# Performance work log

Hardware: AMD Instinct MI355X
Metric: run time of the kernel (lower is better)

The kernel has to match this reference:

```python
import jax, jax.numpy as jnp
import numpy as np

N_HEAD = 12
SCALING = 0.17677669529663687  # 1/sqrt(head_dim=32)


def setup_inputs() -> dict:
    key = jax.random.key(0)
    ks = jax.random.split(key, 6)
    B, R, C, E = 1, 256, 384, 384
    s = 1.0 / np.sqrt(E)
    return {
        "x": jax.random.normal(ks[0], (B, R, C, E), dtype=jnp.float32),
        "Wq": (jax.random.normal(ks[1], (E, E), dtype=jnp.float32) * s),
        "Wk": (jax.random.normal(ks[2], (E, E), dtype=jnp.float32) * s),
        "Wv": (jax.random.normal(ks[3], (E, E), dtype=jnp.float32) * s),
        "Wq_s": (jax.random.normal(ks[4], (E, E), dtype=jnp.float32) * s),
        "Wk_s": (jax.random.normal(ks[5], (E, E), dtype=jnp.float32) * s),
        "res_mask": jnp.ones((B, C), dtype=jnp.int32),
        "seq_mask": jnp.ones((B, R), dtype=jnp.int32),
    }


def reference(x, Wq, Wk, Wv, Wq_s, Wk_s, res_mask, seq_mask):
    B, R, C, E = x.shape
    H = N_HEAD
    D = E // H
    NEG = jnp.finfo(x.dtype).min

    # ---- SeqWeightAttention: per-column attention over rows, query = row 0 ----
    scale_s = 1.0 / np.sqrt(D)
    msa = jnp.transpose(x, (0, 2, 1, 3))                 # [B,C,R,E]
    q0 = msa[:, :, 0]                                    # [B,C,E]
    Qs = (q0 @ Wq_s).reshape(B, C, 1, H, D)
    Qs = jnp.transpose(Qs, (0, 1, 3, 2, 4)) * scale_s    # [B,C,H,1,D]
    Ks = (msa @ Wk_s).reshape(B, C, R, H, D)
    Ks = jnp.transpose(Ks, (0, 1, 3, 4, 2))              # [B,C,H,D,R]
    QKs = Qs @ Ks                                        # [B,C,H,1,R]
    QKs = jnp.where(seq_mask[:, None, None, None, :] == 0, NEG, QKs)
    sw = jax.nn.softmax(QKs, axis=-1)
    sw = jnp.transpose(sw, (0, 4, 1, 2, 3))              # [B,R,C,H,1]

    # ---- main attention, row-contracted (attn_seq_weight path) ----
    scaling = SCALING / np.sqrt(C)                        # seqlen_scaling=True
    Q = (x @ Wq).reshape(B, R, C, H, D) * scaling * sw    # Q modulated by seq weights
    K = (x @ Wk).reshape(B, R, C, H, D)
    V = (x @ Wv).reshape(B, R, C, H, D)

    QK = jnp.einsum('brihd,brjhd->bhij', Q, K)            # contract rows + head_dim
    rm = res_mask[:, :, None] * res_mask[:, None, :]      # [B,C,C]
    QK = jnp.where(rm[:, None, :, :] == 0, NEG, QK)
    attn = jax.nn.softmax(QK, axis=-1)                    # [B,H,C,C]

    out = jnp.einsum('bhij,brjhd->brihd', attn, V)
    return out.reshape(B, R, C, E)
```

## Files before the change

### kernel.cpp

```cpp
#include <hip/hip_runtime.h>
#include <math.h>
#include <stdint.h>

#define DEV_INLINE __device__ __forceinline__

constexpr int R_ = 256, C_ = 384, E_ = 384, H_ = 12, D_ = 32;
constexpr float NEGF = -3.402823466e38f;

typedef __attribute__((ext_vector_type(4))) float f32x4;
typedef __attribute__((ext_vector_type(8))) short short8;
typedef __attribute__((ext_vector_type(4))) unsigned short u16x4;

constexpr size_t o_qs     = 0;
constexpr size_t o_p      = o_qs + (size_t)C_ * E_;
constexpr size_t o_logits = o_p + (size_t)C_ * H_ * E_;
constexpr size_t o_sw     = o_logits + (size_t)C_ * H_ * R_;
constexpr size_t o_attn   = o_sw + (size_t)C_ * H_ * R_;
constexpr size_t o_q3     = o_attn + (size_t)H_ * C_ * C_;
constexpr size_t SZBIG  = 75497472;
constexpr size_t ob_q3b = o_q3 * 4;
constexpr size_t ob_k3b = ob_q3b + SZBIG;
constexpr size_t ob_v3b = ob_k3b + SZBIG;
constexpr size_t ob_xb  = ob_v3b + SZBIG;
constexpr size_t QKSZ   = 7077888;

DEV_INLINE unsigned short bf16h(float x) {
  unsigned int u = __builtin_bit_cast(unsigned int, x);
  unsigned int r = (u + 0x7FFFu + ((u >> 16) & 1u)) >> 16;
  return (unsigned short)r;
}
DEV_INLINE float waveRedMax(float v) {
#pragma unroll
  for (int o = 32; o > 0; o >>= 1) v = fmaxf(v, __shfl_down(v, o));
  return v;
}
DEV_INLINE float waveRedSum(float v) {
#pragma unroll
  for (int o = 32; o > 0; o >>= 1) v += __shfl_down(v, o);
  return v;
}

DEV_INLINE void gll16(const void* g, void* l) {
  __builtin_amdgcn_global_load_lds(
      reinterpret_cast<__attribute__((address_space(1))) void*>(
          reinterpret_cast<uintptr_t>(g)),
      reinterpret_cast<__attribute__((address_space(3))) void*>(
          reinterpret_cast<uintptr_t>(l)),
      16, 0, 0);
}

template <int ROWS, int UPR, int MASK, int SHIFT>
DEV_INLINE void stageT(const unsigned short* __restrict__ g, int lda,
                       unsigned short* l) {
  int t = threadIdx.x, w = t >> 6, lane = t & 63;
  constexpr int NI = (ROWS * UPR) / 64;
  constexpr int PW = NI / 4;
#pragma unroll
  for (int j = 0; j < PW; ++j) {
    int u0 = (w * PW + j) * 64;
    int u = u0 + lane;
    int row = u / UPR, qp = u % UPR;
    int q = qp ^ ((row >> SHIFT) & MASK);
    gll16(g + (size_t)row * lda + q * 8, l + (size_t)u0 * 8);
  }
}

template <int MASK, int SHIFT>
DEV_INLINE short8 fragLd(const unsigned short* base, int row, int q, int rowShorts) {
  int qp = q ^ ((row >> SHIFT) & MASK);
  return *(const short8*)(base + row * rowShorts + qp * 8);
}

__global__ void k_qs(const float* __restrict__ x, const float* __restrict__ Wq_s,
                     float* __restrict__ ws) {
  int c = blockIdx.x, t = threadIdx.x;
  __shared__ float xl[E_];
  xl[t] = x[(size_t)c * E_ + t];
  __syncthreads();
  float s = 0.f;
#pragma unroll 8
  for (int k = 0; k < E_; ++k) s += xl[k] * Wq_s[(size_t)k * E_ + t];
  ws[o_qs + (size_t)c * E_ + t] = s * 0.17677669529663687f;
}

__global__ void k_p(const float* __restrict__ Wk_s, const float* __restrict__ ws,
                    unsigned short* __restrict__ Pb) {
  int h = blockIdx.x, c = blockIdx.y, t = threadIdx.x;
  __shared__ float q[D_];
  float s = 0.f;
  if (h < 12) {
    if (t < D_) q[t] = ws[o_qs + (size_t)c * E_ + h * D_ + t];
    __syncthreads();
    const float* wrow = &Wk_s[(size_t)t * E_ + h * D_];
#pragma unroll
    for (int d = 0; d < D_; d += 4) {
      float4 w = *(const float4*)&wrow[d];
      s += w.x * q[d] + w.y * q[d + 1] + w.z * q[d + 2] + w.w * q[d + 3];
    }
  }
  Pb[((size_t)c * 16 + h) * 384 + t] = bf16h(s);
}

__global__ __launch_bounds__(256) void k_logits_sm(
    const unsigned short* __restrict__ xb, const unsigned short* __restrict__ Pb,
    const int* __restrict__ seq_mask, float* __restrict__ swT) {
  int c = blockIdx.x, t = threadIdx.x;
  __shared__ unsigned short sA[256 * 32];
  __shared__ unsigned short sB[16 * 32];
  __shared__ float lg[12 * 256];
  __shared__ float red[4];
  int w = t >> 6, lane = t & 63, id16 = lane & 15, g = lane >> 4;
  f32x4 acc[4];
#pragma unroll
  for (int mi = 0; mi < 4; ++mi) acc[mi] = (f32x4){0.f, 0.f, 0.f, 0.f};

  for (int k0 = 0; k0 < 384; k0 += 32) {
    stageT<256, 4, 3, 0>(xb + (size_t)c * 384 + k0, 384 * 384, sA);
    if (w == 0) {
      int row = lane >> 2, qp = lane & 3, q = qp ^ (row & 3);
      gll16(Pb + ((size_t)c * 16 + row) * 384 + k0 + q * 8, sB);
    }
    __syncthreads();
    short8 Bf = fragLd<3, 0>(sB, id16, g, 32);
#pragma unroll
    for (int mi = 0; mi < 4; ++mi) {
      short8 Af = fragLd<3, 0>(sA, w * 64 + mi * 16 + id16, g, 32);
      acc[mi] = __builtin_amdgcn_mfma_f32_16x16x32_bf16(Af, Bf, acc[mi], 0, 0, 0);
    }
    __syncthreads();
  }
  int l4 = (lane >> 4) * 4;
#pragma unroll
  for (int mi = 0; mi < 4; ++mi) {
    if (id16 < 12) {
      f32x4 a = acc[mi];
#pragma unroll
      for (int reg = 0; reg < 4; ++reg)
        lg[id16 * 256 + w * 64 + mi * 16 + l4 + reg] = a[reg];
    }
  }
  __syncthreads();
  int wid = t >> 6;
  const float scal = 0.17677669529663687f / sqrtf((float)C_);
  bool masked = (seq_mask[t] == 0);
  for (int h = 0; h < 12; ++h) {
    float v = masked ? NEGF : lg[h * 256 + t];
    float m = waveRedMax(v);
    if ((t & 63) == 0) red[wid] = m;
    __syncthreads();
    float mx = fmaxf(fmaxf(red[0], red[1]), fmaxf(red[2], red[3]));
    __syncthreads();
    float e = expf(v - mx);
    float s = waveRedSum(e);
    if ((t & 63) == 0) red[wid] = s;
    __syncthreads();
    float sum = red[0] + red[1] + red[2] + red[3];
    swT[((size_t)h * 256 + t) * 384 + c] = e / sum * scal;
    __syncthreads();
  }
}

__global__ void k_cvt_x(const float* __restrict__ x, unsigned short* __restrict__ xb) {
  size_t i = ((size_t)blockIdx.x * 256 + threadIdx.x) * 16;
  unsigned short h[16];
#pragma unroll
  for (int j = 0; j < 4; ++j) {
    float4 f = *(const float4*)&x[i + j * 4];
    h[j * 4 + 0] = bf16h(f.x);
    h[j * 4 + 1] = bf16h(f.y);
    h[j * 4 + 2] = bf16h(f.z);
    h[j * 4 + 3] = bf16h(f.w);
  }
  *(short8*)&xb[i] = *(const short8*)&h[0];
  *(short8*)&xb[i + 8] = *(const short8*)&h[8];
}

__global__ void k_cvt_w(const float* __restrict__ Wq, const float* __restrict__ Wk,
                        const float* __restrict__ Wv, unsigned short* __restrict__ Wtb) {
  int n = blockIdx.x, k = threadIdx.x;
  const float* W;
  int col;
  if (n < 384)      { W = Wq; col = n; }
  else if (n < 768) { W = Wk; col = n - 384; }
  else              { W = Wv; col = n - 768; }
  Wtb[(size_t)n * 384 + k] = bf16h(W[(size_t)k * 384 + col]);
}

__global__ __launch_bounds__(256, 4) void k_proj_all(
    const unsigned short* __restrict__ xb, const unsigned short* __restrict__ Wtb,
    const float* __restrict__ swT, unsigned short* __restrict__ Q3b,
    unsigned short* __restrict__ K3b, unsigned short* __restrict__ V3b) {
  __shared__ __align__(16) unsigned short smem[2 * 128 * 64];
  unsigned short* sA = smem;
  unsigned short* sB = smem + 128 * 64;
  int Dd = blockIdx.x;
  int L = (Dd & 7) * 864 + (Dd >> 3);
  int bm = L / 9, bn = L - bm * 9;
  int n0 = bn * 128, m0 = bm * 128;
  int wave = threadIdx.x >> 6, wr = wave >> 1, wc = wave & 1;
  int lane = threadIdx.x & 63, id16 = lane & 15, g = lane >> 4;
  f32x4 acc[4][4];
#pragma unroll
  for (int mi = 0; mi < 4; ++mi)
#pragma unroll
    for (int ni = 0; ni < 4; ++ni) acc[mi][ni] = (f32x4){0.f, 0.f, 0.f, 0.f};

  for (int it = 0; it < 6; ++it) {
    stageT<128, 8, 7, 0>(xb + (size_t)m0 * 384 + it * 64, 384, sA);
    stageT<128, 8, 7, 0>(Wtb + (size_t)n0 * 384 + it * 64, 384, sB);
    __syncthreads();
    short8 Af[4][2], Bf[4][2];
#pragma unroll
    for (int mi = 0; mi < 4; ++mi) {
      int row = wr * 64 + mi * 16 + id16;
#pragma unroll
      for (int kk = 0; kk < 2; ++kk) Af[mi][kk] = fragLd<7, 0>(sA, row, kk * 4 + g, 64);
    }
#pragma unroll
    for (int ni = 0; ni < 4; ++ni) {
      int col = wc * 64 + ni * 16 + id16;
#pragma unroll
      for (int kk = 0; kk < 2; ++kk) Bf[ni][kk] = fragLd<7, 0>(sB, col, kk * 4 + g, 64);
    }
#pragma unroll
    for (int kk = 0; kk < 2; ++kk)
#pragma unroll
      for (int mi = 0; mi < 4; ++mi)
#pragma unroll
        for (int ni = 0; ni < 4; ++ni)
          acc[mi][ni] = __builtin_amdgcn_mfma_f32_16x16x32_bf16(Af[mi][kk], Bf[ni][kk],
                                                                acc[mi][ni], 0, 0, 0);
    __syncthreads();
  }

  int l4 = (lane >> 4) * 4;
  int r = bm / 3, cb = (bm % 3) * 128;
  if (bn < 6) {
    bool isQ = bn < 3;
    int hbase = isQ ? bn * 4 : (bn - 3) * 4;
#pragma unroll
    for (int mi = 0; mi < 4; ++mi) {
      int clBase = wr * 64 + mi * 16 + l4;
#pragma unroll
      for (int ni = 0; ni < 4; ++ni) {
        int nl = wc * 64 + ni * 16 + id16;
        int hhl = nl >> 5, d = nl & 31;
        f32x4 a = acc[mi][ni];
        if (isQ) {
          float4 sv =
              *(const float4*)&swT[((size_t)(hbase + hhl) * 256 + r) * 384 + cb + clBase];
          a[0] *= sv.x; a[1] *= sv.y; a[2] *= sv.z; a[3] *= sv.w;
        }
#pragma unroll
        for (int reg = 0; reg < 4; ++reg)
          smem[hhl * 4096 + (clBase + reg) * 32 + d] = bf16h(a[reg]);
      }
    }
    __syncthreads();
    unsigned short* dst = isQ ? Q3b : K3b;
#pragma unroll
    for (int seg = 0; seg < 8; ++seg) {
      int off = seg * 2048 + threadIdx.x * 8;
      int hhl = off >> 12, inner = off & 4095;
      int hg = hbase + hhl;
      *(short8*)(dst + (((size_t)hg * 256 + r) * 384 + cb) * 32 + inner) =
          *(const short8*)(smem + off);
    }
  } else {
#pragma unroll
    for (int mi = 0; mi < 4; ++mi) {
      int c0 = cb + wr * 64 + mi * 16 + l4;
#pragma unroll
      for (int ni = 0; ni < 4; ++ni) {
        int nv = n0 + wc * 64 + ni * 16 + id16 - 768;
        int hh = nv >> 5, dd = nv & 31;
        f32x4 a = acc[mi][ni];
        u16x4 hv;
#pragma unroll
        for (int reg = 0; reg < 4; ++reg) hv[reg] = bf16h(a[reg]);
        *(u16x4*)(V3b + ((size_t)hh * 8192 + r * 32 + dd) * 384 + c0) = hv;
      }
    }
  }
}

__global__ __launch_bounds__(256, 4) void k_qk_mma(
    const unsigned short* __restrict__ Q3b, const unsigned short* __restrict__ K3b,
    float* __restrict__ QKf0, float* __restrict__ QKf1,
    float* __restrict__ QKf2, float* __restrict__ QKf3) {
  __shared__ unsigned short sA[2 * 4096], sB[2 * 4096];
  int Dd = blockIdx.x;
  int L = (Dd & 7) * 54 + (Dd >> 3);
  int kh = L / 108, rem = L - kh * 108;
  int h = rem / 9, r2 = rem - h * 9, bi = r2 / 3, bj = r2 - bi * 3;
  int i0 = bi * 128, j0 = bj * 128;
  int wave = threadIdx.x >> 6, wr = wave >> 1, wc = wave & 1;
  int lane = threadIdx.x & 63, id16 = lane & 15, g = lane >> 4;
  f32x4 acc[4][4];
#pragma unroll
  for (int mi = 0; mi < 4; ++mi)
#pragma unroll
    for (int ni = 0; ni < 4; ++ni) acc[mi][ni] = (f32x4){0.f, 0.f, 0.f, 0.f};

  for (int it = 0; it < 32; ++it) {
    int r = kh * 64 + it * 2;
#pragma unroll
    for (int rr = 0; rr < 2; ++rr) {
      stageT<128, 4, 3, 1>(Q3b + (((size_t)h * 256 + r + rr) * 384 + i0) * 32, 32,
                           sA + rr * 4096);
      stageT<128, 4, 3, 1>(K3b + (((size_t)h * 256 + r + rr) * 384 + j0) * 32, 32,
                           sB + rr * 4096);
    }
    __syncthreads();
#pragma unroll
    for (int rr = 0; rr < 2; ++rr) {
      short8 Af[4], Bf[4];
#pragma unroll
      for (int mi = 0; mi < 4; ++mi)
        Af[mi] = fragLd<3, 1>(sA + rr * 4096, wr * 64 + mi * 16 + id16, g, 32);
#pragma unroll
      for (int ni = 0; ni < 4; ++ni)
        Bf[ni] = fragLd<3, 1>(sB + rr * 4096, wc * 64 + ni * 16 + id16, g, 32);
#pragma unroll
      for (int mi = 0; mi < 4; ++mi)
#pragma unroll
        for (int ni = 0; ni < 4; ++ni)
          acc[mi][ni] = __builtin_amdgcn_mfma_f32_16x16x32_bf16(Af[mi], Bf[ni],
                                                                acc[mi][ni], 0, 0, 0);
    }
    __syncthreads();
  }
  int l4 = (lane >> 4) * 4;
  float* dst = (kh == 0) ? QKf0 : (kh == 1) ? QKf1 : (kh == 2) ? QKf2 : QKf3;
#pragma unroll
  for (int mi = 0; mi < 4; ++mi)
#pragma unroll
    for (int ni = 0; ni < 4; ++ni) {
      int ii = i0 + wr * 64 + mi * 16 + l4;
      int j = j0 + wc * 64 + ni * 16 + id16;
      f32x4 a = acc[mi][ni];
#pragma unroll
      for (int reg = 0; reg < 4; ++reg)
        dst[((size_t)h * 384 + ii + reg) * 384 + j] = a[reg];
    }
}

__global__ void k_softmax_j(const int* __restrict__ res_mask, const float* __restrict__ QKf0,
                            const float* __restrict__ QKf1, const float* __restrict__ QKf2,
                            const float* __restrict__ QKf3,
                            unsigned short* __restrict__ attnb) {
  int i = blockIdx.x, h = blockIdx.y, t = threadIdx.x;
  int lane = t & 63, wid = t >> 6;
  size_t base = ((size_t)h * C_ + i) * C_;
  float v = (QKf0[base + t] + QKf1[base + t]) + (QKf2[base + t] + QKf3[base + t]);
  if ((res_mask[i] * res_mask[t]) == 0) v = NEGF;
  __shared__ float red[6];
  float m = waveRedMax(v);
  if (lane == 0) red[wid] = m;
  __syncthreads();
  float mx = red[0];
#pragma unroll
  for (int w = 1; w < 6; ++w) mx = fmaxf(mx, red[w]);
  __syncthreads();
  float e = expf(v - mx);
  float s = waveRedSum(e);
  if (lane == 0) red[wid] = s;
  __syncthreads();
  float sum = 0.f;
#pragma unroll
  for (int w = 0; w < 6; ++w) sum += red[w];
  attnb[base + t] = bf16h(e / sum);
}

__global__ __launch_bounds__(256, 4) void k_out_mma(
    const unsigned short* __restrict__ attnb, const unsigned short* __restrict__ V3b,
    float* __restrict__ out) {
  __shared__ __align__(16) unsigned short smem[2 * 128 * 64];
  unsigned short* sA = smem;
  unsigned short* sB = smem + 128 * 64;
  int Dd = blockIdx.x;
  int L = (Dd & 7) * 288 + (Dd >> 3);
  int bn = L % 64, bm = (L / 64) % 3, h = L / 192;
  int n0 = bn * 128, m0 = bm * 128;
  int wave = threadIdx.x >> 6, wr = wave >> 1, wc = wave & 1;
  int lane = threadIdx.x & 63, id16 = lane & 15, g = lane >> 4;
  f32x4 acc[4][4];
#pragma unroll
  for (int mi = 0; mi < 4; ++mi)
#pragma unroll
    for (int ni = 0; ni < 4; ++ni) acc[mi][ni] = (f32x4){0.f, 0.f, 0.f, 0.f};
  const unsigned short* Ab = attnb + (size_t)h * 384 * 384 + (size_t)m0 * 384;
  const unsigned short* Bb = V3b + (size_t)h * 8192 * 384 + (size_t)n0 * 384;

  for (int it = 0; it < 6; ++it) {
    stageT<128, 8, 7, 0>(Ab + it * 64, 384, sA);
    stageT<128, 8, 7, 0>(Bb + it * 64, 384, sB);
    __syncthreads();
    short8 Af[4][2], Bf[4][2];
#pragma unroll
    for (int mi = 0; mi < 4; ++mi) {
      int row = wr * 64 + mi * 16 + id16;
#pragma unroll
      for (int kk = 0; kk < 2; ++kk) Af[mi][kk] = fragLd<7, 0>(sA, row, kk * 4 + g, 64);
    }
#pragma unroll
    for (int ni = 0; ni < 4; ++ni) {
      int col = wc * 64 + ni * 16 + id16;
#pragma unroll
      for (int kk = 0; kk < 2; ++kk) Bf[ni][kk] = fragLd<7, 0>(sB, col, kk * 4 + g, 64);
    }
#pragma unroll
    for (int kk = 0; kk < 2; ++kk)
#pragma unroll
      for (int mi = 0; mi < 4; ++mi)
#pragma unroll
        for (int ni = 0; ni < 4; ++ni)
          acc[mi][ni] = __builtin_amdgcn_mfma_f32_16x16x32_bf16(Af[mi][kk], Bf[ni][kk],
                                                                acc[mi][ni], 0, 0, 0);
    __syncthreads();
  }

  int l4 = (lane >> 4) * 4;
  float* smf = (float*)smem;
#pragma unroll
  for (int p = 0; p < 2; ++p) {
#pragma unroll
    for (int mi = 0; mi < 4; ++mi) {
      int iL = wr * 64 + mi * 16 + l4;
#pragma unroll
      for (int nq = 0; nq < 2; ++nq) {
        int ni = 2 * p + nq;
        int d = nq * 16 + id16;
        f32x4 a = acc[mi][ni];
#pragma unroll
        for (int reg = 0; reg < 4; ++reg)
          smf[wc * 4096 + (iL + reg) * 32 + d] = a[reg];
      }
    }
    __syncthreads();
#pragma unroll
    for (int seg = 0; seg < 8; ++seg) {
      int o = seg * 1024 + threadIdx.x * 4;
      int plane = o >> 12, rest = o & 4095;
      int iL = rest >> 5, d = rest & 31;
      int rg = (n0 >> 5) + plane * 2 + p;
      *(float4*)&out[(((size_t)rg * 384 + m0 + iL) * 12 + h) * 32 + d] =
          *(const float4*)&smf[o];
    }
    __syncthreads();
  }
}

extern "C" void kernel_launch(void* const* d_in, const int* in_sizes, int n_in,
                              void* d_out, int out_size, void* d_ws, size_t ws_size,
                              hipStream_t stream) {
  const float* x = (const float*)d_in[0];
  const float* Wq = (const float*)d_in[1];
  const float* Wk = (const float*)d_in[2];
  const float* Wv = (const float*)d_in[3];
  const float* Wq_s = (const float*)d_in[4];
  const float* Wk_s = (const float*)d_in[5];
  const int* res_mask = (const int*)d_in[6];
  const int* seq_mask = (const int*)d_in[7];
  float* ws = (float*)d_ws;
  char* wsb = (char*)d_ws;
  float* out = (float*)d_out;

  unsigned short* Pb  = (unsigned short*)(wsb + o_p * 4);
  float* swT          = ws + o_logits;
  unsigned short* Wtb = (unsigned short*)(wsb + o_attn * 4);
  float* QKf0         = ws + o_attn;
  unsigned short* Q3b = (unsigned short*)(wsb + ob_q3b);
  unsigned short* K3b = (unsigned short*)(wsb + ob_k3b);
  unsigned short* V3b = (unsigned short*)(wsb + ob_v3b);
  unsigned short* xb  = (unsigned short*)(wsb + ob_xb);
  unsigned short* attnb = Q3b;
  float* QKf1 = (float*)(wsb + ob_xb);
  float* QKf2 = (float*)(wsb + ob_xb + QKSZ);
  float* QKf3 = (float*)(wsb + ob_xb + 2 * QKSZ);

  hipLaunchKernelGGL(k_cvt_x, dim3(9216), dim3(256), 0, stream, x, xb);
  hipLaunchKernelGGL(k_qs, dim3(C_), dim3(E_), 0, stream, x, Wq_s, ws);
  hipLaunchKernelGGL(k_p, dim3(16, C_), dim3(E_), 0, stream, Wk_s, ws, Pb);
  hipLaunchKernelGGL(k_logits_sm, dim3(C_), dim3(256), 0, stream, xb, Pb, seq_mask, swT);
  hipLaunchKernelGGL(k_cvt_w, dim3(1152), dim3(384), 0, stream, Wq, Wk, Wv, Wtb);
  hipLaunchKernelGGL(k_proj_all, dim3(6912), dim3(256), 0, stream, xb, Wtb, swT,
                     Q3b, K3b, V3b);
  hipLaunchKernelGGL(k_qk_mma, dim3(432), dim3(256), 0, stream, Q3b, K3b,
                     QKf0, QKf1, QKf2, QKf3);
  hipLaunchKernelGGL(k_softmax_j, dim3(C_, H_), dim3(C_), 0, stream, res_mask,
                     QKf0, QKf1, QKf2, QKf3, attnb);
  hipLaunchKernelGGL(k_out_mma, dim3(2304), dim3(256), 0, stream, attnb, V3b, out);
}
```

Measured before the change: 373.1 us.

## Double-buffer LDS staging in projection, QK and output MFMA GEMM kernels

Converts the three bf16 MFMA GEMM kernels from a load-sync-compute-sync loop to a two-stage ping-pong LDS pipeline. The next K-slice is staged into the alternate buffer while the current one feeds the MFMAs, so each iteration needs one barrier instead of two. The projection and output kernels go from 64-wide K steps to 32-wide steps with twice as many iterations, which raises loop and barrier overhead per FLOP. Staging is still synchronous global-to-LDS copies issued by the same threads, so the overlap depends on the compiler interleaving loads with MFMA work.

```diff
diff --git a/kernel.cpp b/kernel.cpp
--- a/kernel.cpp
+++ b/kernel.cpp
@@ -190,9 +190,9 @@
     const unsigned short* __restrict__ xb, const unsigned short* __restrict__ Wtb,
     const float* __restrict__ swT, unsigned short* __restrict__ Q3b,
     unsigned short* __restrict__ K3b, unsigned short* __restrict__ V3b) {
-  __shared__ __align__(16) unsigned short smem[2 * 128 * 64];
-  unsigned short* sA = smem;
-  unsigned short* sB = smem + 128 * 64;
+  __shared__ __align__(16) unsigned short smem[16384];
+  unsigned short* sAb[2] = {smem, smem + 4096};
+  unsigned short* sBb[2] = {smem + 8192, smem + 12288};
   int Dd = blockIdx.x;
   int L = (Dd & 7) * 864 + (Dd >> 3);
   int bm = L / 9, bn = L - bm * 9;
@@ -205,31 +205,28 @@
 #pragma unroll
     for (int ni = 0; ni < 4; ++ni) acc[mi][ni] = (f32x4){0.f, 0.f, 0.f, 0.f};
 
-  for (int it = 0; it < 6; ++it) {
-    stageT<128, 8, 7, 0>(xb + (size_t)m0 * 384 + it * 64, 384, sA);
-    stageT<128, 8, 7, 0>(Wtb + (size_t)n0 * 384 + it * 64, 384, sB);
-    __syncthreads();
-    short8 Af[4][2], Bf[4][2];
-#pragma unroll
-    for (int mi = 0; mi < 4; ++mi) {
-      int row = wr * 64 + mi * 16 + id16;
-#pragma unroll
-      for (int kk = 0; kk < 2; ++kk) Af[mi][kk] = fragLd<7, 0>(sA, row, kk * 4 + g, 64);
-    }
-#pragma unroll
-    for (int ni = 0; ni < 4; ++ni) {
-      int col = wc * 64 + ni * 16 + id16;
-#pragma unroll
-      for (int kk = 0; kk < 2; ++kk) Bf[ni][kk] = fragLd<7, 0>(sB, col, kk * 4 + g, 64);
-    }
-#pragma unroll
-    for (int kk = 0; kk < 2; ++kk)
-#pragma unroll
-      for (int mi = 0; mi < 4; ++mi)
-#pragma unroll
-        for (int ni = 0; ni < 4; ++ni)
-          acc[mi][ni] = __builtin_amdgcn_mfma_f32_16x16x32_bf16(Af[mi][kk], Bf[ni][kk],
-                                                                acc[mi][ni], 0, 0, 0);
+  stageT<128, 4, 3, 1>(xb + (size_t)m0 * 384, 384, sAb[0]);
+  stageT<128, 4, 3, 1>(Wtb + (size_t)n0 * 384, 384, sBb[0]);
+  __syncthreads();
+  for (int it = 0; it < 12; ++it) {
+    int cur = it & 1;
+    if (it < 11) {
+      stageT<128, 4, 3, 1>(xb + (size_t)m0 * 384 + (it + 1) * 32, 384, sAb[cur ^ 1]);
+      stageT<128, 4, 3, 1>(Wtb + (size_t)n0 * 384 + (it + 1) * 32, 384, sBb[cur ^ 1]);
+    }
+    short8 Af[4], Bf[4];
+#pragma unroll
+    for (int mi = 0; mi < 4; ++mi)
+      Af[mi] = fragLd<3, 1>(sAb[cur], wr * 64 + mi * 16 + id16, g, 32);
+#pragma unroll
+    for (int ni = 0; ni < 4; ++ni)
+      Bf[ni] = fragLd<3, 1>(sBb[cur], wc * 64 + ni * 16 + id16, g, 32);
+#pragma unroll
+    for (int mi = 0; mi < 4; ++mi)
+#pragma unroll
+      for (int ni = 0; ni < 4; ++ni)
+        acc[mi][ni] = __builtin_amdgcn_mfma_f32_16x16x32_bf16(Af[mi], Bf[ni],
+                                                              acc[mi][ni], 0, 0, 0);
     __syncthreads();
   }
 
@@ -288,7 +285,7 @@
     const unsigned short* __restrict__ Q3b, const unsigned short* __restrict__ K3b,
     float* __restrict__ QKf0, float* __restrict__ QKf1,
     float* __restrict__ QKf2, float* __restrict__ QKf3) {
-  __shared__ unsigned short sA[2 * 4096], sB[2 * 4096];
+  __shared__ unsigned short sA[2][4096], sB[2][4096];
   int Dd = blockIdx.x;
   int L = (Dd & 7) * 54 + (Dd >> 3);
   int kh = L / 108, rem = L - kh * 108;
@@ -301,33 +298,33 @@
   for (int mi = 0; mi < 4; ++mi)
 #pragma unroll
     for (int ni = 0; ni < 4; ++ni) acc[mi][ni] = (f32x4){0.f, 0.f, 0.f, 0.f};
-
-  for (int it = 0; it < 32; ++it) {
-    int r = kh * 64 + it * 2;
-#pragma unroll
-    for (int rr = 0; rr < 2; ++rr) {
-      stageT<128, 4, 3, 1>(Q3b + (((size_t)h * 256 + r + rr) * 384 + i0) * 32, 32,
-                           sA + rr * 4096);
-      stageT<128, 4, 3, 1>(K3b + (((size_t)h * 256 + r + rr) * 384 + j0) * 32, 32,
-                           sB + rr * 4096);
-    }
-    __syncthreads();
-#pragma unroll
-    for (int rr = 0; rr < 2; ++rr) {
-      short8 Af[4], Bf[4];
-#pragma unroll
-      for (int mi = 0; mi < 4; ++mi)
-        Af[mi] = fragLd<3, 1>(sA + rr * 4096, wr * 64 + mi * 16 + id16, g, 32);
+  int rbase = kh * 64;
+
+  stageT<128, 4, 3, 1>(Q3b + (((size_t)h * 256 + rbase) * 384 + i0) * 32, 32, sA[0]);
+  stageT<128, 4, 3, 1>(K3b + (((size_t)h * 256 + rbase) * 384 + j0) * 32, 32, sB[0]);
+  __syncthreads();
+  for (int it = 0; it < 64; ++it) {
+    int cur = it & 1;
+    if (it < 63) {
+      int r = rbase + it + 1;
+      stageT<128, 4, 3, 1>(Q3b + (((size_t)h * 256 + r) * 384 + i0) * 32, 32,
+                           sA[cur ^ 1]);
+      stageT<128, 4, 3, 1>(K3b + (((size_t)h * 256 + r) * 384 + j0) * 32, 32,
+                           sB[cur ^ 1]);
+    }
+    short8 Af[4], Bf[4];
+#pragma unroll
+    for (int mi = 0; mi < 4; ++mi)
+      Af[mi] = fragLd<3, 1>(sA[cur], wr * 64 + mi * 16 + id16, g, 32);
+#pragma unroll
+    for (int ni = 0; ni < 4; ++ni)
+      Bf[ni] = fragLd<3, 1>(sB[cur], wc * 64 + ni * 16 + id16, g, 32);
+#pragma unroll
+    for (int mi = 0; mi < 4; ++mi)
 #pragma unroll
       for (int ni = 0; ni < 4; ++ni)
-        Bf[ni] = fragLd<3, 1>(sB + rr * 4096, wc * 64 + ni * 16 + id16, g, 32);
-#pragma unroll
-      for (int mi = 0; mi < 4; ++mi)
-#pragma unroll
-        for (int ni = 0; ni < 4; ++ni)
-          acc[mi][ni] = __builtin_amdgcn_mfma_f32_16x16x32_bf16(Af[mi], Bf[ni],
-                                                                acc[mi][ni], 0, 0, 0);
-    }
+        acc[mi][ni] = __builtin_amdgcn_mfma_f32_16x16x32_bf16(Af[mi], Bf[ni],
+                                                              acc[mi][ni], 0, 0, 0);
     __syncthreads();
   }
   int l4 = (lane >> 4) * 4;
@@ -375,9 +372,9 @@
 __global__ __launch_bounds__(256, 4) void k_out_mma(
     const unsigned short* __restrict__ attnb, const unsigned short* __restrict__ V3b,
     float* __restrict__ out) {
-  __shared__ __align__(16) unsigned short smem[2 * 128 * 64];
-  unsigned short* sA = smem;
-  unsigned short* sB = smem + 128 * 64;
+  __shared__ __align__(16) unsigned short smem[16384];
+  unsigned short* sAb[2] = {smem, smem + 4096};
+  unsigned short* sBb[2] = {smem + 8192, smem + 12288};
   int Dd = blockIdx.x;
   int L = (Dd & 7) * 288 + (Dd >> 3);
   int bn = L % 64, bm = (L / 64) % 3, h = L / 192;
@@ -392,31 +389,28 @@
   const unsigned short* Ab = attnb + (size_t)h * 384 * 384 + (size_t)m0 * 384;
   const unsigned short* Bb = V3b + (size_t)h * 8192 * 384 + (size_t)n0 * 384;
 
-  for (int it = 0; it < 6; ++it) {
-    stageT<128, 8, 7, 0>(Ab + it * 64, 384, sA);
-    stageT<128, 8, 7, 0>(Bb + it * 64, 384, sB);
-    __syncthreads();
-    short8 Af[4][2], Bf[4][2];
-#pragma unroll
-    for (int mi = 0; mi < 4; ++mi) {
-      int row = wr * 64 + mi * 16 + id16;
-#pragma unroll
-      for (int kk = 0; kk < 2; ++kk) Af[mi][kk] = fragLd<7, 0>(sA, row, kk * 4 + g, 64);
-    }
-#pragma unroll
-    for (int ni = 0; ni < 4; ++ni) {
-      int col = wc * 64 + ni * 16 + id16;
-#pragma unroll
-      for (int kk = 0; kk < 2; ++kk) Bf[ni][kk] = fragLd<7, 0>(sB, col, kk * 4 + g, 64);
-    }
-#pragma unroll
-    for (int kk = 0; kk < 2; ++kk)
-#pragma unroll
-      for (int mi = 0; mi < 4; ++mi)
-#pragma unroll
-        for (int ni = 0; ni < 4; ++ni)
-          acc[mi][ni] = __builtin_amdgcn_mfma_f32_16x16x32_bf16(Af[mi][kk], Bf[ni][kk],
-                                                                acc[mi][ni], 0, 0, 0);
+  stageT<128, 4, 3, 1>(Ab, 384, sAb[0]);
+  stageT<128, 4, 3, 1>(Bb, 384, sBb[0]);
+  __syncthreads();
+  for (int it = 0; it < 12; ++it) {
+    int cur = it & 1;
+    if (it < 11) {
+      stageT<128, 4, 3, 1>(Ab + (it + 1) * 32, 384, sAb[cur ^ 1]);
+      stageT<128, 4, 3, 1>(Bb + (it + 1) * 32, 384, sBb[cur ^ 1]);
+    }
+    short8 Af[4], Bf[4];
+#pragma unroll
+    for (int mi = 0; mi < 4; ++mi)
+      Af[mi] = fragLd<3, 1>(sAb[cur], wr * 64 + mi * 16 + id16, g, 32);
+#pragma unroll
+    for (int ni = 0; ni < 4; ++ni)
+      Bf[ni] = fragLd<3, 1>(sBb[cur], wc * 64 + ni * 16 + id16, g, 32);
+#pragma unroll
+    for (int mi = 0; mi < 4; ++mi)
+#pragma unroll
+      for (int ni = 0; ni < 4; ++ni)
+        acc[mi][ni] = __builtin_amdgcn_mfma_f32_16x16x32_bf16(Af[mi], Bf[ni],
+                                                              acc[mi][ni], 0, 0, 0);
     __syncthreads();
   }
 
```

Result: slower. 390.4 us (+4.7%).

## Merge prep kernels, fold seq-query projection into logits kernel, stage V stores via LDS

Applied to the files above, without the earlier changes.

Combines the x and weight bf16 conversion kernels into one launch. Moves the row-0 query projection and its per-head key projection into the logits kernel, computed in shared memory, which removes two launches and the global Pb round trip. The V output of the projection kernel is now transposed through swizzled LDS so global writes are contiguous along columns rather than scattered 8-byte stores. The logits blocks now do a serial 384x384 scalar matvec per column, which may lengthen that kernel.

```diff
diff --git a/kernel.cpp b/kernel.cpp
--- a/kernel.cpp
+++ b/kernel.cpp
@@ -71,57 +71,76 @@
   return *(const short8*)(base + row * rowShorts + qp * 8);
 }
 
-__global__ void k_qs(const float* __restrict__ x, const float* __restrict__ Wq_s,
-                     float* __restrict__ ws) {
-  int c = blockIdx.x, t = threadIdx.x;
-  __shared__ float xl[E_];
-  xl[t] = x[(size_t)c * E_ + t];
-  __syncthreads();
-  float s = 0.f;
-#pragma unroll 8
-  for (int k = 0; k < E_; ++k) s += xl[k] * Wq_s[(size_t)k * E_ + t];
-  ws[o_qs + (size_t)c * E_ + t] = s * 0.17677669529663687f;
-}
-
-__global__ void k_p(const float* __restrict__ Wk_s, const float* __restrict__ ws,
-                    unsigned short* __restrict__ Pb) {
-  int h = blockIdx.x, c = blockIdx.y, t = threadIdx.x;
-  __shared__ float q[D_];
-  float s = 0.f;
-  if (h < 12) {
-    if (t < D_) q[t] = ws[o_qs + (size_t)c * E_ + h * D_ + t];
-    __syncthreads();
-    const float* wrow = &Wk_s[(size_t)t * E_ + h * D_];
-#pragma unroll
-    for (int d = 0; d < D_; d += 4) {
-      float4 w = *(const float4*)&wrow[d];
-      s += w.x * q[d] + w.y * q[d + 1] + w.z * q[d + 2] + w.w * q[d + 3];
-    }
-  }
-  Pb[((size_t)c * 16 + h) * 384 + t] = bf16h(s);
+__global__ void k_prep(const float* __restrict__ x, const float* __restrict__ Wq,
+                       const float* __restrict__ Wk, const float* __restrict__ Wv,
+                       unsigned short* __restrict__ xb, unsigned short* __restrict__ Wtb) {
+  int bid = blockIdx.x, t = threadIdx.x;
+  if (bid < 6144) {
+    size_t i = ((size_t)bid * 384 + t) * 16;
+    unsigned short h[16];
+#pragma unroll
+    for (int j = 0; j < 4; ++j) {
+      float4 f = *(const float4*)&x[i + j * 4];
+      h[j * 4 + 0] = bf16h(f.x);
+      h[j * 4 + 1] = bf16h(f.y);
+      h[j * 4 + 2] = bf16h(f.z);
+      h[j * 4 + 3] = bf16h(f.w);
+    }
+    *(short8*)&xb[i] = *(const short8*)&h[0];
+    *(short8*)&xb[i + 8] = *(const short8*)&h[8];
+  } else {
+    int n = bid - 6144;
+    const float* W;
+    int col;
+    if (n < 384)      { W = Wq; col = n; }
+    else if (n < 768) { W = Wk; col = n - 384; }
+    else              { W = Wv; col = n - 768; }
+    Wtb[(size_t)n * 384 + t] = bf16h(W[(size_t)t * 384 + col]);
+  }
 }
 
 __global__ __launch_bounds__(256) void k_logits_sm(
-    const unsigned short* __restrict__ xb, const unsigned short* __restrict__ Pb,
+    const float* __restrict__ x, const unsigned short* __restrict__ xb,
+    const float* __restrict__ Wq_s, const float* __restrict__ Wk_s,
     const int* __restrict__ seq_mask, float* __restrict__ swT) {
   int c = blockIdx.x, t = threadIdx.x;
+  __shared__ float xq[384], qs_l[384];
+  __shared__ unsigned short pB[16 * 392];
   __shared__ unsigned short sA[256 * 32];
-  __shared__ unsigned short sB[16 * 32];
   __shared__ float lg[12 * 256];
   __shared__ float red[4];
   int w = t >> 6, lane = t & 63, id16 = lane & 15, g = lane >> 4;
+
+  for (int k = t; k < 384; k += 256) xq[k] = x[(size_t)c * 384 + k];
+  __syncthreads();
+  for (int e = t; e < 384; e += 256) {
+    float s = 0.f;
+    for (int k = 0; k < 384; ++k) s += xq[k] * Wq_s[(size_t)k * 384 + e];
+    qs_l[e] = s * 0.17677669529663687f;
+  }
+  __syncthreads();
+  for (int idx = t; idx < 4608; idx += 256) {
+    int h = idx / 384, kk = idx - h * 384;
+    const float* wrow = &Wk_s[(size_t)kk * 384 + h * 32];
+    const float* qv = &qs_l[h * 32];
+    float s = 0.f;
+#pragma unroll
+    for (int d = 0; d < 32; d += 4) {
+      float4 wv = *(const float4*)&wrow[d];
+      s += wv.x * qv[d] + wv.y * qv[d + 1] + wv.z * qv[d + 2] + wv.w * qv[d + 3];
+    }
+    pB[h * 392 + kk] = bf16h(s);
+  }
+  for (int i = t + 12 * 392; i < 16 * 392; i += 256) pB[i] = 0;
+  __syncthreads();
+
   f32x4 acc[4];
 #pragma unroll
   for (int mi = 0; mi < 4; ++mi) acc[mi] = (f32x4){0.f, 0.f, 0.f, 0.f};
-
   for (int k0 = 0; k0 < 384; k0 += 32) {
     stageT<256, 4, 3, 0>(xb + (size_t)c * 384 + k0, 384 * 384, sA);
-    if (w == 0) {
-      int row = lane >> 2, qp = lane & 3, q = qp ^ (row & 3);
-      gll16(Pb + ((size_t)c * 16 + row) * 384 + k0 + q * 8, sB);
-    }
-    __syncthreads();
-    short8 Bf = fragLd<3, 0>(sB, id16, g, 32);
+    __syncthreads();
+    short8 Bf = *(const short8*)(pB + id16 * 392 + k0 + g * 8);
 #pragma unroll
     for (int mi = 0; mi < 4; ++mi) {
       short8 Af = fragLd<3, 0>(sA, w * 64 + mi * 16 + id16, g, 32);
@@ -158,32 +177,6 @@
     swT[((size_t)h * 256 + t) * 384 + c] = e / sum * scal;
     __syncthreads();
   }
-}
-
-__global__ void k_cvt_x(const float* __restrict__ x, unsigned short* __restrict__ xb) {
-  size_t i = ((size_t)blockIdx.x * 256 + threadIdx.x) * 16;
-  unsigned short h[16];
-#pragma unroll
-  for (int j = 0; j < 4; ++j) {
-    float4 f = *(const float4*)&x[i + j * 4];
-    h[j * 4 + 0] = bf16h(f.x);
-    h[j * 4 + 1] = bf16h(f.y);
-    h[j * 4 + 2] = bf16h(f.z);
-    h[j * 4 + 3] = bf16h(f.w);
-  }
-  *(short8*)&xb[i] = *(const short8*)&h[0];
-  *(short8*)&xb[i + 8] = *(const short8*)&h[8];
-}
-
-__global__ void k_cvt_w(const float* __restrict__ Wq, const float* __restrict__ Wk,
-                        const float* __restrict__ Wv, unsigned short* __restrict__ Wtb) {
-  int n = blockIdx.x, k = threadIdx.x;
-  const float* W;
-  int col;
-  if (n < 384)      { W = Wq; col = n; }
-  else if (n < 768) { W = Wk; col = n - 384; }
-  else              { W = Wv; col = n - 768; }
-  Wtb[(size_t)n * 384 + k] = bf16h(W[(size_t)k * 384 + col]);
 }
 
 __global__ __launch_bounds__(256, 4) void k_proj_all(
@@ -267,19 +260,31 @@
           *(const short8*)(smem + off);
     }
   } else {
-#pragma unroll
-    for (int mi = 0; mi < 4; ++mi) {
-      int c0 = cb + wr * 64 + mi * 16 + l4;
+    int hbase = (bn - 6) * 4;
+#pragma unroll
+    for (int mi = 0; mi < 4; ++mi) {
+      int clBase = wr * 64 + mi * 16 + l4;
 #pragma unroll
       for (int ni = 0; ni < 4; ++ni) {
-        int nv = n0 + wc * 64 + ni * 16 + id16 - 768;
-        int hh = nv >> 5, dd = nv & 31;
+        int nl = wc * 64 + ni * 16 + id16;
+        int hhl = nl >> 5, d = nl & 31;
+        int cg = clBase ^ ((d & 7) << 2);
         f32x4 a = acc[mi][ni];
         u16x4 hv;
 #pragma unroll
         for (int reg = 0; reg < 4; ++reg) hv[reg] = bf16h(a[reg]);
-        *(u16x4*)(V3b + ((size_t)hh * 8192 + r * 32 + dd) * 384 + c0) = hv;
+        *(u16x4*)(smem + hhl * 4096 + d * 128 + cg) = hv;
       }
+    }
+    __syncthreads();
+#pragma unroll
+    for (int seg = 0; seg < 16; ++seg) {
+      int Lg = seg * 1024 + threadIdx.x * 4;
+      int hhl = Lg >> 12, rem = Lg & 4095, d = rem >> 7, cc = rem & 127;
+      int cp = cc ^ ((d & 7) << 2);
+      u16x4 v = *(const u16x4*)(smem + hhl * 4096 + d * 128 + cp);
+      int hg = hbase + hhl;
+      *(u16x4*)(V3b + ((size_t)hg * 8192 + r * 32 + d) * 384 + cb + cc) = v;
     }
   }
 }
@@ -466,7 +471,6 @@
   char* wsb = (char*)d_ws;
   float* out = (float*)d_out;
 
-  unsigned short* Pb  = (unsigned short*)(wsb + o_p * 4);
   float* swT          = ws + o_logits;
   unsigned short* Wtb = (unsigned short*)(wsb + o_attn * 4);
   float* QKf0         = ws + o_attn;
@@ -479,11 +483,9 @@
   float* QKf2 = (float*)(wsb + ob_xb + QKSZ);
   float* QKf3 = (float*)(wsb + ob_xb + 2 * QKSZ);
 
-  hipLaunchKernelGGL(k_cvt_x, dim3(9216), dim3(256), 0, stream, x, xb);
-  hipLaunchKernelGGL(k_qs, dim3(C_), dim3(E_), 0, stream, x, Wq_s, ws);
-  hipLaunchKernelGGL(k_p, dim3(16, C_), dim3(E_), 0, stream, Wk_s, ws, Pb);
-  hipLaunchKernelGGL(k_logits_sm, dim3(C_), dim3(256), 0, stream, xb, Pb, seq_mask, swT);
-  hipLaunchKernelGGL(k_cvt_w, dim3(1152), dim3(384), 0, stream, Wq, Wk, Wv, Wtb);
+  hipLaunchKernelGGL(k_prep, dim3(7296), dim3(384), 0, stream, x, Wq, Wk, Wv, xb, Wtb);
+  hipLaunchKernelGGL(k_logits_sm, dim3(C_), dim3(256), 0, stream, x, xb, Wq_s, Wk_s,
+                     seq_mask, swT);
   hipLaunchKernelGGL(k_proj_all, dim3(6912), dim3(256), 0, stream, xb, Wtb, swT,
                      Q3b, K3b, V3b);
   hipLaunchKernelGGL(k_qk_mma, dim3(432), dim3(256), 0, stream, Q3b, K3b,
```

After: 358.5 us. -3.9%, faster.
